# Kernel optimization log

Measured on AMD Instinct MI355X. Metric: run time of the kernel, lower is better.

Reference implementation:

```python
import jax, jax.numpy as jnp
import numpy as np

B, T, I, O, M = 64, 512, 256, 1024, 8
MS = O // M          # module_size
IM = I * M           # input_dim * num_modules


def setup_inputs() -> dict:
    key = jax.random.key(0)
    ks = jax.random.split(key, 6)
    s = 0.02
    return {
        "x": jax.random.normal(ks[0], (B, T, I), dtype=jnp.float32),
        "W_in": jax.random.normal(ks[1], (O, I), dtype=jnp.float32) * s,
        "b_in": jnp.zeros((O,), dtype=jnp.float32),
        "W_h": jax.random.normal(ks[2], (O, O), dtype=jnp.float32) * s,
        "W_ir": jax.random.normal(ks[3], (IM, I), dtype=jnp.float32) * s,
        "b_ir": jnp.zeros((IM,), dtype=jnp.float32),
        "W_hr": jax.random.normal(ks[4], (IM, IM), dtype=jnp.float32) * s,
        "module_periods": jnp.ones((M,), dtype=jnp.float32),
        "module_shifts": jnp.zeros((M,), dtype=jnp.float32),
    }


def reference(x, W_in, b_in, W_h, W_ir, b_ir, W_hr, module_periods, module_shifts):
    # x: [B, T, I]
    def step(carry, inp):
        h, x_pred = carry           # h: [B,O], x_pred: [B,IM]
        ti, xi = inp                # ti scalar float, xi: [B,I]
        acts = jnp.tanh(xi @ W_in.T + b_in + h @ W_h.T)            # [B,O]
        acts_rec = jnp.tanh(xi @ W_ir.T + b_ir + x_pred @ W_hr.T)  # [B,IM]
        m_xp = x_pred.reshape(B, M, I)
        # NOTE: nn.LogSoftmax() with no dim on a 3D tensor defaults to dim=0 (batch axis)
        surprisal = jax.nn.log_softmax(m_xp, axis=0) * xi[:, None, :]  # [B,M,I]
        mean_surprisal = surprisal.mean(-1)                            # [B,M]
        mp = mean_surprisal * module_periods                           # [B,M]
        gate = (jnp.sin(ti * mp + module_shifts) + 1.0) * 0.5          # [B,M]
        gate_full = jnp.repeat(gate, MS, axis=-1)                      # [B,O]
        y = (1.0 - gate_full) * acts + gate_full * h
        return (y, acts_rec), (y, mp)

    ts = jnp.arange(T, dtype=x.dtype)
    carry0 = (jnp.zeros((B, O), dtype=x.dtype), jnp.zeros((B, IM), dtype=x.dtype))
    (h_final, _), (ys, ps) = jax.lax.scan(step, carry0, (ts, jnp.swapaxes(x, 0, 1)))
    ys = jnp.swapaxes(ys, 0, 1)   # [B,T,O]
    ps = jnp.swapaxes(ps, 0, 1)   # [B,T,M]
    return ys, h_final, ps
```

## Files before the change

kernel.cpp:

```cpp
#include <hip/hip_runtime.h>
#include <hip/hip_fp16.h>

typedef _Float16 f16;
typedef f16 f16x8 __attribute__((ext_vector_type(8)));
typedef f16 f16x4 __attribute__((ext_vector_type(4)));
typedef float f32x4 __attribute__((ext_vector_type(4)));
typedef float f32x16 __attribute__((ext_vector_type(16)));

#define B_ 64
#define T_ 512
#define I_ 256
#define O_ 1024
#define M_ 8
#define IM_ 2048
#define NRECB 128
#define NB 192
#define THREADS 256

#define OFF_X16 4096ull
#define SZ_X16  ((unsigned long long)T_ * B_ * I_ * 2)
#define OFF_XP3 (OFF_X16 + SZ_X16)
#define SZ_XP3  (3ull * B_ * IM_ * 2)
#define OFF_H2  (OFF_XP3 + SZ_XP3)

#define LEAFA(i) ((i) * 16)
#define CENTA    128
#define FLAGA(i) (192 + (i) * 16)
#define LEAFB(i) (320 + (i) * 16)
#define CENTB    448
#define FLAGB(i) (512 + (i) * 16)

#define CMB_REC 147456
#define XPRAW   81920
#define CMB_ACT 114688
#define LSE_O   126976
#define PART_O  128000
#define GATE_O  129024
#define SMEM_SZ 159744

#define WAITV(N) asm volatile("s_waitcnt vmcnt(" #N ")" ::: "memory")
#define LGKM0    asm volatile("s_waitcnt lgkmcnt(0)" ::: "memory")
#define SCHEDB   __builtin_amdgcn_sched_barrier(0)
#define BARRIER  __builtin_amdgcn_s_barrier()

#define ISSUE_AX(BUF, P) asm volatile( \
    "global_load_dwordx4 %0, %8, off\n\t" \
    "global_load_dwordx4 %1, %8, off offset:32\n\t" \
    "global_load_dwordx4 %2, %8, off offset:64\n\t" \
    "global_load_dwordx4 %3, %8, off offset:96\n\t" \
    "global_load_dwordx4 %4, %8, off offset:128\n\t" \
    "global_load_dwordx4 %5, %8, off offset:160\n\t" \
    "global_load_dwordx4 %6, %8, off offset:192\n\t" \
    "global_load_dwordx4 %7, %8, off offset:224" \
    : "=&v"(abuf[BUF][0]), "=&v"(abuf[BUF][1]), "=&v"(abuf[BUF][2]), "=&v"(abuf[BUF][3]), \
      "=&v"(abuf[BUF][4]), "=&v"(abuf[BUF][5]), "=&v"(abuf[BUF][6]), "=&v"(abuf[BUF][7]) \
    : "v"(P) : "memory")

#define ISSUE_AS(BUF, P) asm volatile( \
    "global_load_dwordx4 %0, %8, off sc0 sc1\n\t" \
    "global_load_dwordx4 %1, %8, off offset:32 sc0 sc1\n\t" \
    "global_load_dwordx4 %2, %8, off offset:64 sc0 sc1\n\t" \
    "global_load_dwordx4 %3, %8, off offset:96 sc0 sc1\n\t" \
    "global_load_dwordx4 %4, %8, off offset:128 sc0 sc1\n\t" \
    "global_load_dwordx4 %5, %8, off offset:160 sc0 sc1\n\t" \
    "global_load_dwordx4 %6, %8, off offset:192 sc0 sc1\n\t" \
    "global_load_dwordx4 %7, %8, off offset:224 sc0 sc1" \
    : "=&v"(abuf[BUF][0]), "=&v"(abuf[BUF][1]), "=&v"(abuf[BUF][2]), "=&v"(abuf[BUF][3]), \
      "=&v"(abuf[BUF][4]), "=&v"(abuf[BUF][5]), "=&v"(abuf[BUF][6]), "=&v"(abuf[BUF][7]) \
    : "v"(P) : "memory")

#define ISSUE8P(ARR, P0,P1,P2,P3,P4,P5,P6,P7) asm volatile( \
    "global_load_dwordx4 %0, %8, off sc0 sc1\n\t" \
    "global_load_dwordx4 %1, %9, off sc0 sc1\n\t" \
    "global_load_dwordx4 %2, %10, off sc0 sc1\n\t" \
    "global_load_dwordx4 %3, %11, off sc0 sc1\n\t" \
    "global_load_dwordx4 %4, %12, off sc0 sc1\n\t" \
    "global_load_dwordx4 %5, %13, off sc0 sc1\n\t" \
    "global_load_dwordx4 %6, %14, off sc0 sc1\n\t" \
    "global_load_dwordx4 %7, %15, off sc0 sc1" \
    : "=&v"((ARR)[0]), "=&v"((ARR)[1]), "=&v"((ARR)[2]), "=&v"((ARR)[3]), \
      "=&v"((ARR)[4]), "=&v"((ARR)[5]), "=&v"((ARR)[6]), "=&v"((ARR)[7]) \
    : "v"(P0), "v"(P1), "v"(P2), "v"(P3), "v"(P4), "v"(P5), "v"(P6), "v"(P7) \
    : "memory")

#define CH(I, WN) do { \
    WAITV(WN); SCHEDB; \
    _Pragma("unroll") \
    for (int kb = 0; kb < 8; ++kb) { \
        f16x8 bf = *(const f16x8*)(smem + addrB[kb] + (I) * 256); \
        if (kb & 1) acc1 = __builtin_amdgcn_mfma_f32_32x32x16_f16(abuf[I][kb], bf, acc1, 0, 0, 0); \
        else        acc0 = __builtin_amdgcn_mfma_f32_32x32x16_f16(abuf[I][kb], bf, acc0, 0, 0, 0); \
    } \
} while (0)

__device__ __forceinline__ void st_coh_h(f16* p, float vf) {
    union { f16 h; short s; } u; u.h = (f16)vf;
    asm volatile("global_store_short %0, %1, off sc0 sc1" :: "v"(p), "v"((int)u.s) : "memory");
}

__device__ __forceinline__ float fast_tanh(float x) {
    float e = __expf(2.f * x);
    return 1.f - 2.f / (e + 1.f);
}

__device__ __forceinline__ unsigned ld_rlx(unsigned* p) {
    return __hip_atomic_load(p, __ATOMIC_RELAXED, __HIP_MEMORY_SCOPE_AGENT);
}

__device__ __forceinline__ void post_flags(unsigned* bar, int base, unsigned v) {
    #pragma unroll
    for (int i = 0; i < 8; ++i) {
        unsigned* rp = &bar[base + i * 16];
        asm volatile("global_store_dword %0, %1, off sc0 sc1" :: "v"(rp), "v"(v) : "memory");
    }
}

__device__ __forceinline__ void arriveA(unsigned* bar, int blk, int t) {
    unsigned old = __hip_atomic_fetch_add(&bar[LEAFA(blk & 7)], 1u, __ATOMIC_RELAXED, __HIP_MEMORY_SCOPE_AGENT);
    if (old % 16u == 15u) {
        unsigned r = __hip_atomic_fetch_add(&bar[CENTA], 1u, __ATOMIC_RELAXED, __HIP_MEMORY_SCOPE_AGENT);
        if ((r & 7u) == 7u) post_flags(bar, FLAGA(0), (unsigned)(t + 1));
    }
}
__device__ __forceinline__ void arriveB(unsigned* bar, int a, int t) {
    unsigned old = __hip_atomic_fetch_add(&bar[LEAFB(a & 7)], 1u, __ATOMIC_RELAXED, __HIP_MEMORY_SCOPE_AGENT);
    if ((old & 7u) == 7u) {
        unsigned r = __hip_atomic_fetch_add(&bar[CENTB], 1u, __ATOMIC_RELAXED, __HIP_MEMORY_SCOPE_AGENT);
        if ((r & 7u) == 7u) post_flags(bar, FLAGB(0), (unsigned)(t + 1));
    }
}

__global__ void init_kernel(const float* __restrict__ x, char* __restrict__ ws) {
    const int gid = blockIdx.x * 256 + threadIdx.x;
    if (blockIdx.x == 0) {
        for (int i = threadIdx.x; i < 1024; i += 256) ((unsigned*)ws)[i] = 0u;
    }
    f16* x16 = (f16*)(ws + OFF_X16);
    const int NQ = T_ * B_ * (I_ / 4);
    for (int q = gid; q < NQ; q += 256 * 256) {
        int t = q >> 12;
        int rem = q & 4095;
        int b = rem >> 6;
        int k4 = rem & 63;
        f32x4 v = *(const f32x4*)(x + ((size_t)b * T_ + t) * I_ + k4 * 4);
        f16x4 h;
        h[0] = (f16)v[0]; h[1] = (f16)v[1]; h[2] = (f16)v[2]; h[3] = (f16)v[3];
        *(f16x4*)(x16 + ((size_t)t * B_ + b) * I_ + k4 * 4) = h;
    }
    f16x8 z = {0, 0, 0, 0, 0, 0, 0, 0};
    f16* xp0 = (f16*)(ws + OFF_XP3);
    for (int e = gid * 8; e < B_ * IM_; e += 256 * 256 * 8) *(f16x8*)(xp0 + e) = z;
    f16* h0 = (f16*)(ws + OFF_H2);
    for (int e = gid * 8; e < B_ * O_; e += 256 * 256 * 8) *(f16x8*)(h0 + e) = z;
}

__global__ __launch_bounds__(THREADS, 1) void cwrnn_kernel(
    const float* __restrict__ x, const float* __restrict__ W_in, const float* __restrict__ b_in,
    const float* __restrict__ W_h, const float* __restrict__ W_ir, const float* __restrict__ b_ir,
    const float* __restrict__ W_hr, const float* __restrict__ periods, const float* __restrict__ shifts,
    float* __restrict__ out, char* __restrict__ ws)
{
    __shared__ __align__(16) char smem[SMEM_SZ];

    unsigned* bar = (unsigned*)ws;
    const int blk = blockIdx.x, tid = threadIdx.x;
    const int lane = tid & 63, w = tid >> 6;
    const int col = lane & 31, g = lane >> 5;

    float* ys = out;
    float* hfin = out + (size_t)B_ * T_ * O_;
    float* ps = hfin + (size_t)B_ * O_;

    if (blk < NRECB) {
        const int cg = blk >> 1, rh = blk & 1;
        const int j0 = cg * 32;
        const int row0 = rh * 32;
        const int arow = row0 + col;
        {
            const int j = tid & 31;
            const float* ra = W_ir + (size_t)(j0 + j) * I_;
            const float* rb = W_hr + (size_t)(j0 + j) * IM_ - 256;
            for (int u = (tid >> 5); u < 288; u += 8) {
                int k0 = u * 8;
                const float* s = (k0 < 256) ? (ra + k0) : (rb + k0);
                f32x4 lo = *(const f32x4*)s;
                f32x4 hi = *(const f32x4*)(s + 4);
                f16x8 v;
                #pragma unroll
                for (int e = 0; e < 4; ++e) { v[e] = (f16)lo[e]; v[e + 4] = (f16)hi[e]; }
                *(f16x8*)(smem + j * 4608 + ((u ^ (j & 15)) << 4)) = v;
            }
        }
        const float bir = b_ir[j0 + col];
        LGKM0; BARRIER;

        const int c0k = (w == 0) ? 0 : (w == 1) ? 5 : (w == 2) ? 10 : 14;
        int addrB[8];
        #pragma unroll
        for (int kb = 0; kb < 8; ++kb)
            addrB[kb] = col * 4608 + ((((kb << 1) + g) ^ (col & 15)) << 4) + c0k * 256;

        const char* xrow0 = (const char*)(ws + OFF_X16) + (size_t)arow * 512 + g * 16;
        f16* const xpB = (f16*)(ws + OFF_XP3);
        unsigned* fA = &bar[FLAGA(blk & 7)];
        unsigned* fB = &bar[FLAGB(blk & 7)];

        for (int t = 0; t < T_ - 1; ++t) {
            if (tid == 0) {
                while (1) {
                    int fa = (int)ld_rlx(fA);
                    int fb = (int)ld_rlx(fB);
                    if (fa >= t && fb >= t - 1) break;
                    __builtin_amdgcn_s_sleep(2);
                }
            }
            BARRIER;
            const int bi = t % 3;
            int bn = bi + 1; if (bn == 3) bn = 0;
            const f16* xpcur = xpB + (size_t)bi * B_ * IM_;
            f16* xpnxt = xpB + (size_t)bn * B_ * IM_;
            const char* sprow = (const char*)xpcur + (size_t)arow * 4096 + g * 16 - 512;
            const char* xrow = xrow0 + (size_t)t * 32768;

            f16x8 abuf[5][8];
            f32x16 acc0, acc1;
            #pragma unroll
            for (int r = 0; r < 16; ++r) { acc0[r] = 0.f; acc1[r] = 0.f; }

            if (w == 0) {
                ISSUE_AX(0, xrow); ISSUE_AX(1, (xrow + 256));
                ISSUE_AS(2, (sprow + 2 * 256)); ISSUE_AS(3, (sprow + 3 * 256)); ISSUE_AS(4, (sprow + 4 * 256));
                CH(0, 32); CH(1, 24); CH(2, 16); CH(3, 8); CH(4, 0);
            } else if (w == 1) {
                ISSUE_AS(0, (sprow + 5 * 256)); ISSUE_AS(1, (sprow + 6 * 256)); ISSUE_AS(2, (sprow + 7 * 256));
                ISSUE_AS(3, (sprow + 8 * 256)); ISSUE_AS(4, (sprow + 9 * 256));
                CH(0, 32); CH(1, 24); CH(2, 16); CH(3, 8); CH(4, 0);
            } else if (w == 2) {
                ISSUE_AS(0, (sprow + 10 * 256)); ISSUE_AS(1, (sprow + 11 * 256));
                ISSUE_AS(2, (sprow + 12 * 256)); ISSUE_AS(3, (sprow + 13 * 256));
                CH(0, 24); CH(1, 16); CH(2, 8); CH(3, 0);
            } else {
                ISSUE_AS(0, (sprow + 14 * 256)); ISSUE_AS(1, (sprow + 15 * 256));
                ISSUE_AS(2, (sprow + 16 * 256)); ISSUE_AS(3, (sprow + 17 * 256));
                CH(0, 24); CH(1, 16); CH(2, 8); CH(3, 0);
            }

            f32x16 accS;
            #pragma unroll
            for (int r = 0; r < 16; ++r) accS[r] = acc0[r] + acc1[r];
            if (w > 0) {
                char* cb = smem + CMB_REC + (w - 1) * 4096 + lane * 16;
                #pragma unroll
                for (int q = 0; q < 4; ++q) {
                    f32x4 v = { accS[q*4+0], accS[q*4+1], accS[q*4+2], accS[q*4+3] };
                    *(f32x4*)(cb + q * 1024) = v;
                }
            }
            LGKM0; BARRIER;
            if (w == 0) {
                #pragma unroll
                for (int wv = 0; wv < 3; ++wv) {
                    const char* cb = smem + CMB_REC + wv * 4096 + lane * 16;
                    #pragma unroll
                    for (int q = 0; q < 4; ++q) {
                        f32x4 v = *(const f32x4*)(cb + q * 1024);
                        accS[q*4+0] += v[0]; accS[q*4+1] += v[1];
                        accS[q*4+2] += v[2]; accS[q*4+3] += v[3];
                    }
                }
                #pragma unroll
                for (int r = 0; r < 16; ++r) {
                    int rloc = (r & 3) + ((r >> 2) << 3) + (g << 2);
                    st_coh_h(xpnxt + (size_t)(row0 + rloc) * IM_ + j0 + col, fast_tanh(accS[r] + bir));
                }
            }
            WAITV(0);
            BARRIER;
            if (tid == 0) arriveA(bar, blk, t);
        }
    } else {
        const int a = blk - NRECB;
        const int colg = a >> 1, rh = a & 1;
        const int m = colg >> 2;
        const int o0 = colg * 32;
        const int row0 = rh * 32;
        const int arow = row0 + col;
        {
            const int j = tid & 31;
            const float* ra = W_in + (size_t)(o0 + j) * I_;
            const float* rb = W_h + (size_t)(o0 + j) * O_ - 256;
            for (int u = (tid >> 5); u < 160; u += 8) {
                int k0 = u * 8;
                const float* s = (k0 < 256) ? (ra + k0) : (rb + k0);
                f32x4 lo = *(const f32x4*)s;
                f32x4 hi = *(const f32x4*)(s + 4);
                f16x8 v;
                #pragma unroll
                for (int e = 0; e < 4; ++e) { v[e] = (f16)lo[e]; v[e + 4] = (f16)hi[e]; }
                *(f16x8*)(smem + j * 2560 + ((u ^ (j & 15)) << 4)) = v;
            }
        }
        const float bin = b_in[o0 + col];
        const float per = periods[m], shf = shifts[m];
        LGKM0; BARRIER;

        const int c0k = (w == 0) ? 0 : (w == 1) ? 3 : (w == 2) ? 6 : 8;
        int addrB[8];
        #pragma unroll
        for (int kb = 0; kb < 8; ++kb)
            addrB[kb] = col * 2560 + ((((kb << 1) + g) ^ (col & 15)) << 4) + c0k * 256;

        char* xp_raw = smem + XPRAW;
        float* lse_lds = (float*)(smem + LSE_O);
        float* part_lds = (float*)(smem + PART_O);
        float* gate_lds = (float*)(smem + GATE_O);

        const char* xrow0 = (const char*)(ws + OFF_X16) + (size_t)arow * 512 + g * 16;
        const f16* xpB = (const f16*)(ws + OFF_XP3);
        f16* h2 = (f16*)(ws + OFF_H2);
        unsigned* fA = &bar[FLAGA(a & 7)];
        unsigned* fB = &bar[FLAGB(a & 7)];
        float hreg[16];
        #pragma unroll
        for (int r = 0; r < 16; ++r) hreg[r] = 0.f;

        const int s_ = tid - 128;
        const int cg2 = s_ & 31;
        const int r0s = (s_ >> 5) << 4;

        for (int t = 0; t < T_; ++t) {
            if (tid == 0) {
                while (1) {
                    int fa = (int)ld_rlx(fA);
                    int fb = (int)ld_rlx(fB);
                    if (fa >= t && fb >= t) break;
                    __builtin_amdgcn_s_sleep(2);
                }
            }
            BARRIER;
            const int bi = t % 3;
            const f16* xpcur = xpB + (size_t)bi * B_ * IM_;
            const f16* hcur = h2 + (size_t)(t & 1) * B_ * O_;
            f16* hnxt = h2 + (size_t)((t + 1) & 1) * B_ * O_;

            const char* sprow = (const char*)hcur + (size_t)arow * 2048 + g * 16 - 512;
            const char* xrow = xrow0 + (size_t)t * 32768;
            f16x8 abuf[3][8];
            f16x8 sregA[8], sregB[8];
            f32x16 acc0, acc1;
            #pragma unroll
            for (int r = 0; r < 16; ++r) { acc0[r] = 0.f; acc1[r] = 0.f; }

            if (w == 0) {
                ISSUE_AX(0, xrow); ISSUE_AX(1, (xrow + 256)); ISSUE_AS(2, (sprow + 2 * 256));
                CH(0, 16); CH(1, 8); CH(2, 0);
            } else if (w == 1) {
                ISSUE_AS(0, (sprow + 3 * 256)); ISSUE_AS(1, (sprow + 4 * 256)); ISSUE_AS(2, (sprow + 5 * 256));
                CH(0, 16); CH(1, 8); CH(2, 0);
            } else {
                const int ca = (w == 2) ? 6 : 8;
                ISSUE_AS(0, (sprow + ca * 256)); ISSUE_AS(1, (sprow + (ca + 1) * 256));
                const char* xb = (const char*)xpcur + (size_t)m * 512 + (size_t)cg2 * 16 + (size_t)r0s * 4096;
                ISSUE8P(sregA, xb, xb + 4096, xb + 2*4096, xb + 3*4096,
                               xb + 4*4096, xb + 5*4096, xb + 6*4096, xb + 7*4096);
                ISSUE8P(sregB, (xb + 8*4096), xb + 9*4096, xb + 10*4096, xb + 11*4096,
                               xb + 12*4096, xb + 13*4096, xb + 14*4096, xb + 15*4096);
                CH(0, 24); CH(1, 16);
                WAITV(0); SCHEDB;
                #pragma unroll
                for (int k = 0; k < 8; ++k) {
                    int b0 = r0s + k;
                    *(f16x8*)(xp_raw + (size_t)b0 * 512 + ((cg2 ^ (b0 & 7)) << 4)) = sregA[k];
                    int b1 = r0s + 8 + k;
                    *(f16x8*)(xp_raw + (size_t)b1 * 512 + ((cg2 ^ (b1 & 7)) << 4)) = sregB[k];
                }
            }

            f32x16 accS;
            #pragma unroll
            for (int r = 0; r < 16; ++r) accS[r] = acc0[r] + acc1[r];
            if (w > 0) {
                char* cb = smem + CMB_ACT + (w - 1) * 4096 + lane * 16;
                #pragma unroll
                for (int q = 0; q < 4; ++q) {
                    f32x4 v = { accS[q*4+0], accS[q*4+1], accS[q*4+2], accS[q*4+3] };
                    *(f32x4*)(cb + q * 1024) = v;
                }
            }
            LGKM0; BARRIER;
            {
                int i = tid;
                int gq = i >> 3, r2 = (i & 7) * 2;
                float s = 0.f;
                #pragma unroll 8
                for (int b = 0; b < B_; ++b)
                    s += __expf((float)*(const f16*)(xp_raw + b * 512 + ((gq ^ (b & 7)) << 4) + r2));
                lse_lds[i] = __logf(s);
            }
            if (w == 0) {
                #pragma unroll
                for (int wv = 0; wv < 3; ++wv) {
                    const char* cb = smem + CMB_ACT + wv * 4096 + lane * 16;
                    #pragma unroll
                    for (int q = 0; q < 4; ++q) {
                        f32x4 v = *(const f32x4*)(cb + q * 1024);
                        accS[q*4+0] += v[0]; accS[q*4+1] += v[1];
                        accS[q*4+2] += v[2]; accS[q*4+3] += v[3];
                    }
                }
            }
            LGKM0; BARRIER;
            {
                int b = tid >> 2, q = tid & 3;
                const float* xr = x + ((size_t)b * T_ + t) * I_ + q * 64;
                float s = 0.f;
                #pragma unroll
                for (int k = 0; k < 8; ++k) {
                    f16x8 xp8 = *(const f16x8*)(xp_raw + (size_t)b * 512 + ((((q << 3) + k) ^ (b & 7)) << 4));
                    f32x4 xa = *(const f32x4*)(xr + k * 8);
                    f32x4 xb2 = *(const f32x4*)(xr + k * 8 + 4);
                    #pragma unroll
                    for (int jj = 0; jj < 4; ++jj)
                        s += ((float)xp8[jj] - lse_lds[(q << 6) + (k << 3) + jj]) * xa[jj];
                    #pragma unroll
                    for (int jj = 0; jj < 4; ++jj)
                        s += ((float)xp8[jj + 4] - lse_lds[(q << 6) + (k << 3) + 4 + jj]) * xb2[jj];
                }
                part_lds[tid] = s;
            }
            LGKM0; BARRIER;
            if (tid < B_) {
                float s = part_lds[tid * 4] + part_lds[tid * 4 + 1] + part_lds[tid * 4 + 2] + part_lds[tid * 4 + 3];
                float mp = (s * (1.f / 256.f)) * per;
                gate_lds[tid] = 0.5f * (sinf((float)t * mp + shf) + 1.f);
                if ((a & 7) == 0) ps[((size_t)tid * T_ + t) * M_ + m] = mp;
            }
            LGKM0; BARRIER;
            if (w == 0) {
                #pragma unroll
                for (int r = 0; r < 16; ++r) {
                    int rloc = (r & 3) + ((r >> 2) << 3) + (g << 2);
                    int row = row0 + rloc;
                    float gt = gate_lds[row];
                    float av = fast_tanh(accS[r] + bin);
                    float y = (1.f - gt) * av + gt * hreg[r];
                    hreg[r] = y;
                    st_coh_h(hnxt + (size_t)row * O_ + o0 + col, y);
                    ys[((size_t)row * T_ + t) * O_ + o0 + col] = y;
                    if (t == T_ - 1) hfin[(size_t)row * O_ + o0 + col] = y;
                }
            }
            WAITV(0);
            BARRIER;
            if (tid == 0) arriveB(bar, a, t);
        }
    }
}

extern "C" void kernel_launch(void* const* d_in, const int* in_sizes, int n_in,
                              void* d_out, int out_size, void* d_ws, size_t ws_size,
                              hipStream_t stream) {
    const float* x    = (const float*)d_in[0];
    const float* W_in = (const float*)d_in[1];
    const float* b_in = (const float*)d_in[2];
    const float* W_h  = (const float*)d_in[3];
    const float* W_ir = (const float*)d_in[4];
    const float* b_ir = (const float*)d_in[5];
    const float* W_hr = (const float*)d_in[6];
    const float* per  = (const float*)d_in[7];
    const float* shf  = (const float*)d_in[8];

    hipLaunchKernelGGL(init_kernel, dim3(256), dim3(256), 0, stream,
                       x, (char*)d_ws);
    hipLaunchKernelGGL(cwrnn_kernel, dim3(NB), dim3(THREADS), 0, stream,
                       x, W_in, b_in, W_h, W_ir, b_ir, W_hr, per, shf,
                       (float*)d_out, (char*)d_ws);
}
```

Before: 5.471 ms.

## Replicate per-step state into per-XCD buffers to read with L2-cached loads

Each block reads its XCD ID at startup and registers itself, then the blocks on each XCD cooperatively copy the current x_pred and h state into a per-XCD replica buffer every timestep. A per-XCD counter barrier guards the copy. The GEMM operand loads then read the replica with sc0 only instead of sc0 sc1, so they can hit the local L2 rather than going to memory coherently. This adds a copy phase and an extra intra-XCD barrier per step, and the recurrence loop now runs T iterations so recurrent blocks take part in the copying.

```diff
diff --git a/kernel.cpp b/kernel.cpp
--- a/kernel.cpp
+++ b/kernel.cpp
@@ -17,11 +17,13 @@
 #define NB 192
 #define THREADS 256
 
-#define OFF_X16 4096ull
-#define SZ_X16  ((unsigned long long)T_ * B_ * I_ * 2)
-#define OFF_XP3 (OFF_X16 + SZ_X16)
-#define SZ_XP3  (3ull * B_ * IM_ * 2)
-#define OFF_H2  (OFF_XP3 + SZ_XP3)
+#define OFF_X16 8192ull
+#define OFF_XP3 16785408ull
+#define OFF_H2  17571840ull
+#define OFF_REP 17833984ull
+#define REP_XCD 786432ull
+#define REP_PAR 393216ull
+#define REP_H   262144ull
 
 #define LEAFA(i) ((i) * 16)
 #define CENTA    128
@@ -29,6 +31,11 @@
 #define LEAFB(i) (320 + (i) * 16)
 #define CENTB    448
 #define FLAGB(i) (512 + (i) * 16)
+#define REGC     640
+#define NR_(i)   (656 + (i) * 16)
+#define NA_(i)   (784 + (i) * 16)
+#define XBX_(i)  (912 + (i) * 16)
+#define XBH_(i)  (1040 + (i) * 16)
 
 #define CMB_REC 147456
 #define XPRAW   81920
@@ -36,7 +43,8 @@
 #define LSE_O   126976
 #define PART_O  128000
 #define GATE_O  129024
-#define SMEM_SZ 159744
+#define META_O  159744
+#define SMEM_SZ 159808
 
 #define WAITV(N) asm volatile("s_waitcnt vmcnt(" #N ")" ::: "memory")
 #define LGKM0    asm volatile("s_waitcnt lgkmcnt(0)" ::: "memory")
@@ -56,28 +64,28 @@
       "=&v"(abuf[BUF][4]), "=&v"(abuf[BUF][5]), "=&v"(abuf[BUF][6]), "=&v"(abuf[BUF][7]) \
     : "v"(P) : "memory")
 
-#define ISSUE_AS(BUF, P) asm volatile( \
-    "global_load_dwordx4 %0, %8, off sc0 sc1\n\t" \
-    "global_load_dwordx4 %1, %8, off offset:32 sc0 sc1\n\t" \
-    "global_load_dwordx4 %2, %8, off offset:64 sc0 sc1\n\t" \
-    "global_load_dwordx4 %3, %8, off offset:96 sc0 sc1\n\t" \
-    "global_load_dwordx4 %4, %8, off offset:128 sc0 sc1\n\t" \
-    "global_load_dwordx4 %5, %8, off offset:160 sc0 sc1\n\t" \
-    "global_load_dwordx4 %6, %8, off offset:192 sc0 sc1\n\t" \
-    "global_load_dwordx4 %7, %8, off offset:224 sc0 sc1" \
+#define ISSUE_A0(BUF, P) asm volatile( \
+    "global_load_dwordx4 %0, %8, off sc0\n\t" \
+    "global_load_dwordx4 %1, %8, off offset:32 sc0\n\t" \
+    "global_load_dwordx4 %2, %8, off offset:64 sc0\n\t" \
+    "global_load_dwordx4 %3, %8, off offset:96 sc0\n\t" \
+    "global_load_dwordx4 %4, %8, off offset:128 sc0\n\t" \
+    "global_load_dwordx4 %5, %8, off offset:160 sc0\n\t" \
+    "global_load_dwordx4 %6, %8, off offset:192 sc0\n\t" \
+    "global_load_dwordx4 %7, %8, off offset:224 sc0" \
     : "=&v"(abuf[BUF][0]), "=&v"(abuf[BUF][1]), "=&v"(abuf[BUF][2]), "=&v"(abuf[BUF][3]), \
       "=&v"(abuf[BUF][4]), "=&v"(abuf[BUF][5]), "=&v"(abuf[BUF][6]), "=&v"(abuf[BUF][7]) \
     : "v"(P) : "memory")
 
-#define ISSUE8P(ARR, P0,P1,P2,P3,P4,P5,P6,P7) asm volatile( \
-    "global_load_dwordx4 %0, %8, off sc0 sc1\n\t" \
-    "global_load_dwordx4 %1, %9, off sc0 sc1\n\t" \
-    "global_load_dwordx4 %2, %10, off sc0 sc1\n\t" \
-    "global_load_dwordx4 %3, %11, off sc0 sc1\n\t" \
-    "global_load_dwordx4 %4, %12, off sc0 sc1\n\t" \
-    "global_load_dwordx4 %5, %13, off sc0 sc1\n\t" \
-    "global_load_dwordx4 %6, %14, off sc0 sc1\n\t" \
-    "global_load_dwordx4 %7, %15, off sc0 sc1" \
+#define ISSUE8P0(ARR, P0,P1,P2,P3,P4,P5,P6,P7) asm volatile( \
+    "global_load_dwordx4 %0, %8, off sc0\n\t" \
+    "global_load_dwordx4 %1, %9, off sc0\n\t" \
+    "global_load_dwordx4 %2, %10, off sc0\n\t" \
+    "global_load_dwordx4 %3, %11, off sc0\n\t" \
+    "global_load_dwordx4 %4, %12, off sc0\n\t" \
+    "global_load_dwordx4 %5, %13, off sc0\n\t" \
+    "global_load_dwordx4 %6, %14, off sc0\n\t" \
+    "global_load_dwordx4 %7, %15, off sc0" \
     : "=&v"((ARR)[0]), "=&v"((ARR)[1]), "=&v"((ARR)[2]), "=&v"((ARR)[3]), \
       "=&v"((ARR)[4]), "=&v"((ARR)[5]), "=&v"((ARR)[6]), "=&v"((ARR)[7]) \
     : "v"(P0), "v"(P1), "v"(P2), "v"(P3), "v"(P4), "v"(P5), "v"(P6), "v"(P7) \
@@ -106,6 +114,9 @@
 __device__ __forceinline__ unsigned ld_rlx(unsigned* p) {
     return __hip_atomic_load(p, __ATOMIC_RELAXED, __HIP_MEMORY_SCOPE_AGENT);
 }
+__device__ __forceinline__ unsigned rmw_add(unsigned* p) {
+    return __hip_atomic_fetch_add(p, 1u, __ATOMIC_RELAXED, __HIP_MEMORY_SCOPE_AGENT);
+}
 
 __device__ __forceinline__ void post_flags(unsigned* bar, int base, unsigned v) {
     #pragma unroll
@@ -116,24 +127,46 @@
 }
 
 __device__ __forceinline__ void arriveA(unsigned* bar, int blk, int t) {
-    unsigned old = __hip_atomic_fetch_add(&bar[LEAFA(blk & 7)], 1u, __ATOMIC_RELAXED, __HIP_MEMORY_SCOPE_AGENT);
+    unsigned old = rmw_add(&bar[LEAFA(blk & 7)]);
     if (old % 16u == 15u) {
-        unsigned r = __hip_atomic_fetch_add(&bar[CENTA], 1u, __ATOMIC_RELAXED, __HIP_MEMORY_SCOPE_AGENT);
+        unsigned r = rmw_add(&bar[CENTA]);
         if ((r & 7u) == 7u) post_flags(bar, FLAGA(0), (unsigned)(t + 1));
     }
 }
 __device__ __forceinline__ void arriveB(unsigned* bar, int a, int t) {
-    unsigned old = __hip_atomic_fetch_add(&bar[LEAFB(a & 7)], 1u, __ATOMIC_RELAXED, __HIP_MEMORY_SCOPE_AGENT);
+    unsigned old = rmw_add(&bar[LEAFB(a & 7)]);
     if ((old & 7u) == 7u) {
-        unsigned r = __hip_atomic_fetch_add(&bar[CENTB], 1u, __ATOMIC_RELAXED, __HIP_MEMORY_SCOPE_AGENT);
+        unsigned r = rmw_add(&bar[CENTB]);
         if ((r & 7u) == 7u) post_flags(bar, FLAGB(0), (unsigned)(t + 1));
+    }
+}
+
+__device__ __forceinline__ void copy_slices(const char* src, char* dst,
+                                            int r, int c, int nslices, int tid) {
+    for (int s = r; s < nslices; s += c) {
+        const char* p0 = src + (size_t)s * 16384 + tid * 16;
+        char* d0 = dst + (size_t)s * 16384 + tid * 16;
+        f16x8 v0, v1, v2, v3;
+        asm volatile(
+            "global_load_dwordx4 %0, %4, off sc0 sc1\n\t"
+            "global_load_dwordx4 %1, %5, off sc0 sc1\n\t"
+            "global_load_dwordx4 %2, %6, off sc0 sc1\n\t"
+            "global_load_dwordx4 %3, %7, off sc0 sc1"
+            : "=&v"(v0), "=&v"(v1), "=&v"(v2), "=&v"(v3)
+            : "v"(p0), "v"(p0 + 4096), "v"(p0 + 8192), "v"(p0 + 12288)
+            : "memory");
+        WAITV(0); SCHEDB;
+        *(f16x8*)(d0) = v0;
+        *(f16x8*)(d0 + 4096) = v1;
+        *(f16x8*)(d0 + 8192) = v2;
+        *(f16x8*)(d0 + 12288) = v3;
     }
 }
 
 __global__ void init_kernel(const float* __restrict__ x, char* __restrict__ ws) {
     const int gid = blockIdx.x * 256 + threadIdx.x;
     if (blockIdx.x == 0) {
-        for (int i = threadIdx.x; i < 1024; i += 256) ((unsigned*)ws)[i] = 0u;
+        for (int i = threadIdx.x; i < 2048; i += 256) ((unsigned*)ws)[i] = 0u;
     }
     f16* x16 = (f16*)(ws + OFF_X16);
     const int NQ = T_ * B_ * (I_ / 4);
@@ -171,7 +204,37 @@
     float* hfin = out + (size_t)B_ * T_ * O_;
     float* ps = hfin + (size_t)B_ * O_;
 
-    if (blk < NRECB) {
+    int* meta = (int*)(smem + META_O);
+    if (tid == 0) {
+        unsigned xcdv;
+        asm volatile("s_getreg_b32 %0, hwreg(HW_REG_XCC_ID)" : "=s"(xcdv));
+        xcdv &= 7u;
+        unsigned rnk;
+        if (blk < NRECB) rnk = rmw_add(&bar[NR_(xcdv)]);
+        else             rnk = rmw_add(&bar[NA_(xcdv)]);
+        WAITV(0);
+        rmw_add(&bar[REGC]);
+        while (ld_rlx(&bar[REGC]) < (unsigned)NB) __builtin_amdgcn_s_sleep(8);
+        meta[0] = (int)xcdv;
+        meta[1] = (int)rnk;
+        meta[2] = (int)ld_rlx(&bar[NR_(xcdv)]);
+        meta[3] = (int)ld_rlx(&bar[NA_(xcdv)]);
+    }
+    LGKM0; BARRIER;
+    const int xcd = meta[0], rank = meta[1], nR = meta[2], nA = meta[3];
+    const bool isREC = (blk < NRECB);
+    const bool doXP = isREC || (nR == 0);
+    const bool doH  = (!isREC) || (nA == 0);
+    const int cX = (nR > 0) ? nR : nA;
+    const int cH = (nA > 0) ? nA : nR;
+    const bool needFbT = isREC && (nA == 0);
+    char* rep = ws + OFF_REP + (size_t)xcd * REP_XCD;
+    unsigned* xbX = &bar[XBX_(xcd)];
+    unsigned* xbH = &bar[XBH_(xcd)];
+    f16* const xpB = (f16*)(ws + OFF_XP3);
+    f16* h2 = (f16*)(ws + OFF_H2);
+
+    if (isREC) {
         const int cg = blk >> 1, rh = blk & 1;
         const int j0 = cg * 32;
         const int row0 = rh * 32;
@@ -201,80 +264,94 @@
             addrB[kb] = col * 4608 + ((((kb << 1) + g) ^ (col & 15)) << 4) + c0k * 256;
 
         const char* xrow0 = (const char*)(ws + OFF_X16) + (size_t)arow * 512 + g * 16;
-        f16* const xpB = (f16*)(ws + OFF_XP3);
         unsigned* fA = &bar[FLAGA(blk & 7)];
         unsigned* fB = &bar[FLAGB(blk & 7)];
 
-        for (int t = 0; t < T_ - 1; ++t) {
+        for (int t = 0; t < T_; ++t) {
             if (tid == 0) {
                 while (1) {
                     int fa = (int)ld_rlx(fA);
                     int fb = (int)ld_rlx(fB);
-                    if (fa >= t && fb >= t - 1) break;
+                    if (fa >= t && fb >= t - 1 && (!needFbT || fb >= t)) break;
                     __builtin_amdgcn_s_sleep(2);
                 }
             }
             BARRIER;
             const int bi = t % 3;
             int bn = bi + 1; if (bn == 3) bn = 0;
-            const f16* xpcur = xpB + (size_t)bi * B_ * IM_;
-            f16* xpnxt = xpB + (size_t)bn * B_ * IM_;
-            const char* sprow = (const char*)xpcur + (size_t)arow * 4096 + g * 16 - 512;
-            const char* xrow = xrow0 + (size_t)t * 32768;
-
-            f16x8 abuf[5][8];
-            f32x16 acc0, acc1;
-            #pragma unroll
-            for (int r = 0; r < 16; ++r) { acc0[r] = 0.f; acc1[r] = 0.f; }
-
-            if (w == 0) {
-                ISSUE_AX(0, xrow); ISSUE_AX(1, (xrow + 256));
-                ISSUE_AS(2, (sprow + 2 * 256)); ISSUE_AS(3, (sprow + 3 * 256)); ISSUE_AS(4, (sprow + 4 * 256));
-                CH(0, 32); CH(1, 24); CH(2, 16); CH(3, 8); CH(4, 0);
-            } else if (w == 1) {
-                ISSUE_AS(0, (sprow + 5 * 256)); ISSUE_AS(1, (sprow + 6 * 256)); ISSUE_AS(2, (sprow + 7 * 256));
-                ISSUE_AS(3, (sprow + 8 * 256)); ISSUE_AS(4, (sprow + 9 * 256));
-                CH(0, 32); CH(1, 24); CH(2, 16); CH(3, 8); CH(4, 0);
-            } else if (w == 2) {
-                ISSUE_AS(0, (sprow + 10 * 256)); ISSUE_AS(1, (sprow + 11 * 256));
-                ISSUE_AS(2, (sprow + 12 * 256)); ISSUE_AS(3, (sprow + 13 * 256));
-                CH(0, 24); CH(1, 16); CH(2, 8); CH(3, 0);
-            } else {
-                ISSUE_AS(0, (sprow + 14 * 256)); ISSUE_AS(1, (sprow + 15 * 256));
-                ISSUE_AS(2, (sprow + 16 * 256)); ISSUE_AS(3, (sprow + 17 * 256));
-                CH(0, 24); CH(1, 16); CH(2, 8); CH(3, 0);
-            }
-
-            f32x16 accS;
-            #pragma unroll
-            for (int r = 0; r < 16; ++r) accS[r] = acc0[r] + acc1[r];
-            if (w > 0) {
-                char* cb = smem + CMB_REC + (w - 1) * 4096 + lane * 16;
-                #pragma unroll
-                for (int q = 0; q < 4; ++q) {
-                    f32x4 v = { accS[q*4+0], accS[q*4+1], accS[q*4+2], accS[q*4+3] };
-                    *(f32x4*)(cb + q * 1024) = v;
-                }
-            }
-            LGKM0; BARRIER;
-            if (w == 0) {
-                #pragma unroll
-                for (int wv = 0; wv < 3; ++wv) {
-                    const char* cb = smem + CMB_REC + wv * 4096 + lane * 16;
+            char* repP = rep + (size_t)(t & 1) * REP_PAR;
+            if (doXP) copy_slices((const char*)(xpB + (size_t)bi * B_ * IM_), repP, rank, cX, 16, tid);
+            if (doH)  copy_slices((const char*)(h2 + (size_t)(t & 1) * B_ * O_), repP + REP_H, rank, cH, 8, tid);
+            WAITV(0);
+            BARRIER;
+            if (tid == 0) {
+                if (doXP) rmw_add(xbX);
+                if (doH)  rmw_add(xbH);
+            }
+            if (t < T_ - 1) {
+                if (tid == 0) {
+                    unsigned tgt = (unsigned)(cX * (t + 1));
+                    while (ld_rlx(xbX) < tgt) __builtin_amdgcn_s_sleep(1);
+                }
+                BARRIER;
+                f16* xpnxt = xpB + (size_t)bn * B_ * IM_;
+                const char* sprow = (const char*)repP + (size_t)arow * 4096 + g * 16 - 512;
+                const char* xrow = xrow0 + (size_t)t * 32768;
+
+                f16x8 abuf[5][8];
+                f32x16 acc0, acc1;
+                #pragma unroll
+                for (int r = 0; r < 16; ++r) { acc0[r] = 0.f; acc1[r] = 0.f; }
+
+                if (w == 0) {
+                    ISSUE_AX(0, xrow); ISSUE_AX(1, (xrow + 256));
+                    ISSUE_A0(2, (sprow + 2 * 256)); ISSUE_A0(3, (sprow + 3 * 256)); ISSUE_A0(4, (sprow + 4 * 256));
+                    CH(0, 32); CH(1, 24); CH(2, 16); CH(3, 8); CH(4, 0);
+                } else if (w == 1) {
+                    ISSUE_A0(0, (sprow + 5 * 256)); ISSUE_A0(1, (sprow + 6 * 256)); ISSUE_A0(2, (sprow + 7 * 256));
+                    ISSUE_A0(3, (sprow + 8 * 256)); ISSUE_A0(4, (sprow + 9 * 256));
+                    CH(0, 32); CH(1, 24); CH(2, 16); CH(3, 8); CH(4, 0);
+                } else if (w == 2) {
+                    ISSUE_A0(0, (sprow + 10 * 256)); ISSUE_A0(1, (sprow + 11 * 256));
+                    ISSUE_A0(2, (sprow + 12 * 256)); ISSUE_A0(3, (sprow + 13 * 256));
+                    CH(0, 24); CH(1, 16); CH(2, 8); CH(3, 0);
+                } else {
+                    ISSUE_A0(0, (sprow + 14 * 256)); ISSUE_A0(1, (sprow + 15 * 256));
+                    ISSUE_A0(2, (sprow + 16 * 256)); ISSUE_A0(3, (sprow + 17 * 256));
+                    CH(0, 24); CH(1, 16); CH(2, 8); CH(3, 0);
+                }
+
+                f32x16 accS;
+                #pragma unroll
+                for (int r = 0; r < 16; ++r) accS[r] = acc0[r] + acc1[r];
+                if (w > 0) {
+                    char* cb = smem + CMB_REC + (w - 1) * 4096 + lane * 16;
                     #pragma unroll
                     for (int q = 0; q < 4; ++q) {
-                        f32x4 v = *(const f32x4*)(cb + q * 1024);
-                        accS[q*4+0] += v[0]; accS[q*4+1] += v[1];
-                        accS[q*4+2] += v[2]; accS[q*4+3] += v[3];
+                        f32x4 v = { accS[q*4+0], accS[q*4+1], accS[q*4+2], accS[q*4+3] };
+                        *(f32x4*)(cb + q * 1024) = v;
                     }
                 }
-                #pragma unroll
-                for (int r = 0; r < 16; ++r) {
-                    int rloc = (r & 3) + ((r >> 2) << 3) + (g << 2);
-                    st_coh_h(xpnxt + (size_t)(row0 + rloc) * IM_ + j0 + col, fast_tanh(accS[r] + bir));
-                }
-            }
-            WAITV(0);
+                LGKM0; BARRIER;
+                if (w == 0) {
+                    #pragma unroll
+                    for (int wv = 0; wv < 3; ++wv) {
+                        const char* cb = smem + CMB_REC + wv * 4096 + lane * 16;
+                        #pragma unroll
+                        for (int q = 0; q < 4; ++q) {
+                            f32x4 v = *(const f32x4*)(cb + q * 1024);
+                            accS[q*4+0] += v[0]; accS[q*4+1] += v[1];
+                            accS[q*4+2] += v[2]; accS[q*4+3] += v[3];
+                        }
+                    }
+                    #pragma unroll
+                    for (int r = 0; r < 16; ++r) {
+                        int rloc = (r & 3) + ((r >> 2) << 3) + (g << 2);
+                        st_coh_h(xpnxt + (size_t)(row0 + rloc) * IM_ + j0 + col, fast_tanh(accS[r] + bir));
+                    }
+                }
+                WAITV(0);
+            }
             BARRIER;
             if (tid == 0) arriveA(bar, blk, t);
         }
@@ -316,8 +393,6 @@
         float* gate_lds = (float*)(smem + GATE_O);
 
         const char* xrow0 = (const char*)(ws + OFF_X16) + (size_t)arow * 512 + g * 16;
-        const f16* xpB = (const f16*)(ws + OFF_XP3);
-        f16* h2 = (f16*)(ws + OFF_H2);
         unsigned* fA = &bar[FLAGA(a & 7)];
         unsigned* fB = &bar[FLAGB(a & 7)];
         float hreg[16];
@@ -339,11 +414,20 @@
             }
             BARRIER;
             const int bi = t % 3;
-            const f16* xpcur = xpB + (size_t)bi * B_ * IM_;
-            const f16* hcur = h2 + (size_t)(t & 1) * B_ * O_;
+            char* repP = rep + (size_t)(t & 1) * REP_PAR;
+            if (doXP) copy_slices((const char*)(xpB + (size_t)bi * B_ * IM_), repP, rank, cX, 16, tid);
+            if (doH)  copy_slices((const char*)(h2 + (size_t)(t & 1) * B_ * O_), repP + REP_H, rank, cH, 8, tid);
+            WAITV(0);
+            BARRIER;
+            if (tid == 0) {
+                if (doXP) rmw_add(xbX);
+                if (doH)  rmw_add(xbH);
+                unsigned tX = (unsigned)(cX * (t + 1)), tH = (unsigned)(cH * (t + 1));
+                while (ld_rlx(xbX) < tX || ld_rlx(xbH) < tH) __builtin_amdgcn_s_sleep(1);
+            }
+            BARRIER;
             f16* hnxt = h2 + (size_t)((t + 1) & 1) * B_ * O_;
-
-            const char* sprow = (const char*)hcur + (size_t)arow * 2048 + g * 16 - 512;
+            const char* sprow = (const char*)repP + REP_H + (size_t)arow * 2048 + g * 16 - 512;
             const char* xrow = xrow0 + (size_t)t * 32768;
             f16x8 abuf[3][8];
             f16x8 sregA[8], sregB[8];
@@ -352,18 +436,18 @@
             for (int r = 0; r < 16; ++r) { acc0[r] = 0.f; acc1[r] = 0.f; }
 
             if (w == 0) {
-                ISSUE_AX(0, xrow); ISSUE_AX(1, (xrow + 256)); ISSUE_AS(2, (sprow + 2 * 256));
+                ISSUE_AX(0, xrow); ISSUE_AX(1, (xrow + 256)); ISSUE_A0(2, (sprow + 2 * 256));
                 CH(0, 16); CH(1, 8); CH(2, 0);
             } else if (w == 1) {
-                ISSUE_AS(0, (sprow + 3 * 256)); ISSUE_AS(1, (sprow + 4 * 256)); ISSUE_AS(2, (sprow + 5 * 256));
+                ISSUE_A0(0, (sprow + 3 * 256)); ISSUE_A0(1, (sprow + 4 * 256)); ISSUE_A0(2, (sprow + 5 * 256));
                 CH(0, 16); CH(1, 8); CH(2, 0);
             } else {
                 const int ca = (w == 2) ? 6 : 8;
-                ISSUE_AS(0, (sprow + ca * 256)); ISSUE_AS(1, (sprow + (ca + 1) * 256));
-                const char* xb = (const char*)xpcur + (size_t)m * 512 + (size_t)cg2 * 16 + (size_t)r0s * 4096;
-                ISSUE8P(sregA, xb, xb + 4096, xb + 2*4096, xb + 3*4096,
+                ISSUE_A0(0, (sprow + ca * 256)); ISSUE_A0(1, (sprow + (ca + 1) * 256));
+                const char* xb = (const char*)repP + (size_t)m * 512 + (size_t)cg2 * 16 + (size_t)r0s * 4096;
+                ISSUE8P0(sregA, xb, xb + 4096, xb + 2*4096, xb + 3*4096,
                                xb + 4*4096, xb + 5*4096, xb + 6*4096, xb + 7*4096);
-                ISSUE8P(sregB, (xb + 8*4096), xb + 9*4096, xb + 10*4096, xb + 11*4096,
+                ISSUE8P0(sregB, (xb + 8*4096), xb + 9*4096, xb + 10*4096, xb + 11*4096,
                                xb + 12*4096, xb + 13*4096, xb + 14*4096, xb + 15*4096);
                 CH(0, 24); CH(1, 16);
                 WAITV(0); SCHEDB;
```

Result: slower. 6.366 ms (+16.4%).

## Replace atomic tree barriers with per-block flag slots polled by wavefronts

Applied to the files above, without the earlier changes.

Removes the hierarchical atomic-counter barrier (leaf/center counters plus broadcast flags). Each block now writes its own progress flag slot after its stores, and consumers poll only the slots they depend on, with one wave checking 64 slots via ballot. The x_pred ring grows from three to four buffers so recurrent blocks can run further ahead of the activation blocks. This cuts out the atomic round trips and the trailing block-wide barrier on the critical path per timestep, at the cost of more polling traffic and a reliance on the memory ordering of the coherent stores.

```diff
diff --git a/kernel.cpp b/kernel.cpp
--- a/kernel.cpp
+++ b/kernel.cpp
@@ -17,18 +17,13 @@
 #define NB 192
 #define THREADS 256
 
-#define OFF_X16 4096ull
-#define SZ_X16  ((unsigned long long)T_ * B_ * I_ * 2)
-#define OFF_XP3 (OFF_X16 + SZ_X16)
-#define SZ_XP3  (3ull * B_ * IM_ * 2)
-#define OFF_H2  (OFF_XP3 + SZ_XP3)
-
-#define LEAFA(i) ((i) * 16)
-#define CENTA    128
-#define FLAGA(i) (192 + (i) * 16)
-#define LEAFB(i) (320 + (i) * 16)
-#define CENTB    448
-#define FLAGB(i) (512 + (i) * 16)
+#define OFF_X16 16384ull
+#define SZ_X16  16777216ull
+#define OFF_XP4 (OFF_X16 + SZ_X16)
+#define OFF_H2  (OFF_XP4 + 4ull * B_ * IM_ * 2)
+
+#define RECF_D(rh) (1024 + (rh) * 256)
+#define ACTF_D     1536
 
 #define CMB_REC 147456
 #define XPRAW   81920
@@ -103,37 +98,20 @@
     return 1.f - 2.f / (e + 1.f);
 }
 
-__device__ __forceinline__ unsigned ld_rlx(unsigned* p) {
-    return __hip_atomic_load(p, __ATOMIC_RELAXED, __HIP_MEMORY_SCOPE_AGENT);
-}
-
-__device__ __forceinline__ void post_flags(unsigned* bar, int base, unsigned v) {
-    #pragma unroll
-    for (int i = 0; i < 8; ++i) {
-        unsigned* rp = &bar[base + i * 16];
-        asm volatile("global_store_dword %0, %1, off sc0 sc1" :: "v"(rp), "v"(v) : "memory");
-    }
-}
-
-__device__ __forceinline__ void arriveA(unsigned* bar, int blk, int t) {
-    unsigned old = __hip_atomic_fetch_add(&bar[LEAFA(blk & 7)], 1u, __ATOMIC_RELAXED, __HIP_MEMORY_SCOPE_AGENT);
-    if (old % 16u == 15u) {
-        unsigned r = __hip_atomic_fetch_add(&bar[CENTA], 1u, __ATOMIC_RELAXED, __HIP_MEMORY_SCOPE_AGENT);
-        if ((r & 7u) == 7u) post_flags(bar, FLAGA(0), (unsigned)(t + 1));
-    }
-}
-__device__ __forceinline__ void arriveB(unsigned* bar, int a, int t) {
-    unsigned old = __hip_atomic_fetch_add(&bar[LEAFB(a & 7)], 1u, __ATOMIC_RELAXED, __HIP_MEMORY_SCOPE_AGENT);
-    if ((old & 7u) == 7u) {
-        unsigned r = __hip_atomic_fetch_add(&bar[CENTB], 1u, __ATOMIC_RELAXED, __HIP_MEMORY_SCOPE_AGENT);
-        if ((r & 7u) == 7u) post_flags(bar, FLAGB(0), (unsigned)(t + 1));
-    }
+__device__ __forceinline__ int ld_flag(const unsigned* p) {
+    int v;
+    asm volatile("global_load_dword %0, %1, off sc0 sc1" : "=v"(v) : "v"(p) : "memory");
+    WAITV(0);
+    return v;
+}
+__device__ __forceinline__ void st_flag(unsigned* p, int v) {
+    asm volatile("global_store_dword %0, %1, off sc0 sc1" :: "v"(p), "v"(v) : "memory");
 }
 
 __global__ void init_kernel(const float* __restrict__ x, char* __restrict__ ws) {
     const int gid = blockIdx.x * 256 + threadIdx.x;
     if (blockIdx.x == 0) {
-        for (int i = threadIdx.x; i < 1024; i += 256) ((unsigned*)ws)[i] = 0u;
+        for (int i = threadIdx.x; i < 4096; i += 256) ((unsigned*)ws)[i] = 0u;
     }
     f16* x16 = (f16*)(ws + OFF_X16);
     const int NQ = T_ * B_ * (I_ / 4);
@@ -148,7 +126,7 @@
         *(f16x4*)(x16 + ((size_t)t * B_ + b) * I_ + k4 * 4) = h;
     }
     f16x8 z = {0, 0, 0, 0, 0, 0, 0, 0};
-    f16* xp0 = (f16*)(ws + OFF_XP3);
+    f16* xp0 = (f16*)(ws + OFF_XP4);
     for (int e = gid * 8; e < B_ * IM_; e += 256 * 256 * 8) *(f16x8*)(xp0 + e) = z;
     f16* h0 = (f16*)(ws + OFF_H2);
     for (int e = gid * 8; e < B_ * O_; e += 256 * 256 * 8) *(f16x8*)(h0 + e) = z;
@@ -170,6 +148,9 @@
     float* ys = out;
     float* hfin = out + (size_t)B_ * T_ * O_;
     float* ps = hfin + (size_t)B_ * O_;
+
+    f16* const xpB = (f16*)(ws + OFF_XP4);
+    f16* h2 = (f16*)(ws + OFF_H2);
 
     if (blk < NRECB) {
         const int cg = blk >> 1, rh = blk & 1;
@@ -201,22 +182,19 @@
             addrB[kb] = col * 4608 + ((((kb << 1) + g) ^ (col & 15)) << 4) + c0k * 256;
 
         const char* xrow0 = (const char*)(ws + OFF_X16) + (size_t)arow * 512 + g * 16;
-        f16* const xpB = (f16*)(ws + OFF_XP3);
-        unsigned* fA = &bar[FLAGA(blk & 7)];
-        unsigned* fB = &bar[FLAGB(blk & 7)];
+        unsigned* myslot = bar + RECF_D(rh) + cg * 4;
 
         for (int t = 0; t < T_ - 1; ++t) {
-            if (tid == 0) {
-                while (1) {
-                    int fa = (int)ld_rlx(fA);
-                    int fb = (int)ld_rlx(fB);
-                    if (fa >= t && fb >= t - 1) break;
-                    __builtin_amdgcn_s_sleep(2);
-                }
+            if (w == 0) {
+                const unsigned* p = bar + RECF_D(rh) + lane * 4;
+                while (__ballot(ld_flag(p) >= t) != ~0ull) __builtin_amdgcn_s_sleep(4);
+            } else if (w == 1) {
+                const unsigned* p = bar + ACTF_D + lane * 4;
+                const int tgt = t - 2;
+                while (__ballot(ld_flag(p) >= tgt) != ~0ull) __builtin_amdgcn_s_sleep(4);
             }
             BARRIER;
-            const int bi = t % 3;
-            int bn = bi + 1; if (bn == 3) bn = 0;
+            const int bi = t & 3, bn = (t + 1) & 3;
             const f16* xpcur = xpB + (size_t)bi * B_ * IM_;
             f16* xpnxt = xpB + (size_t)bn * B_ * IM_;
             const char* sprow = (const char*)xpcur + (size_t)arow * 4096 + g * 16 - 512;
@@ -273,10 +251,9 @@
                     int rloc = (r & 3) + ((r >> 2) << 3) + (g << 2);
                     st_coh_h(xpnxt + (size_t)(row0 + rloc) * IM_ + j0 + col, fast_tanh(accS[r] + bir));
                 }
-            }
-            WAITV(0);
-            BARRIER;
-            if (tid == 0) arriveA(bar, blk, t);
+                WAITV(0);
+                if (tid == 0) st_flag(myslot, t + 1);
+            }
         }
     } else {
         const int a = blk - NRECB;
@@ -316,10 +293,7 @@
         float* gate_lds = (float*)(smem + GATE_O);
 
         const char* xrow0 = (const char*)(ws + OFF_X16) + (size_t)arow * 512 + g * 16;
-        const f16* xpB = (const f16*)(ws + OFF_XP3);
-        f16* h2 = (f16*)(ws + OFF_H2);
-        unsigned* fA = &bar[FLAGA(a & 7)];
-        unsigned* fB = &bar[FLAGB(a & 7)];
+        unsigned* myslot = bar + ACTF_D + (rh * 32 + colg) * 4;
         float hreg[16];
         #pragma unroll
         for (int r = 0; r < 16; ++r) hreg[r] = 0.f;
@@ -329,16 +303,18 @@
         const int r0s = (s_ >> 5) << 4;
 
         for (int t = 0; t < T_; ++t) {
-            if (tid == 0) {
-                while (1) {
-                    int fa = (int)ld_rlx(fA);
-                    int fb = (int)ld_rlx(fB);
-                    if (fa >= t && fb >= t) break;
-                    __builtin_amdgcn_s_sleep(2);
-                }
+            if (w == 0) {
+                const unsigned* p = bar + RECF_D(0) + lane * 4;
+                while (__ballot(ld_flag(p) >= t) != ~0ull) __builtin_amdgcn_s_sleep(4);
+            } else if (w == 1) {
+                const unsigned* p = bar + RECF_D(1) + lane * 4;
+                while (__ballot(ld_flag(p) >= t) != ~0ull) __builtin_amdgcn_s_sleep(4);
+            } else if (w == 2) {
+                const unsigned* p = bar + ACTF_D + (rh * 32 + (lane & 31)) * 4;
+                while (__ballot((lane < 32) ? (ld_flag(p) >= t) : 1) != ~0ull) __builtin_amdgcn_s_sleep(4);
             }
             BARRIER;
-            const int bi = t % 3;
+            const int bi = t & 3;
             const f16* xpcur = xpB + (size_t)bi * B_ * IM_;
             const f16* hcur = h2 + (size_t)(t & 1) * B_ * O_;
             f16* hnxt = h2 + (size_t)((t + 1) & 1) * B_ * O_;
@@ -449,10 +425,9 @@
                     ys[((size_t)row * T_ + t) * O_ + o0 + col] = y;
                     if (t == T_ - 1) hfin[(size_t)row * O_ + o0 + col] = y;
                 }
-            }
-            WAITV(0);
-            BARRIER;
-            if (tid == 0) arriveB(bar, a, t);
+                WAITV(0);
+                if (tid == 0) st_flag(myslot, t + 1);
+            }
         }
     }
 }
```

Result: no change. 5.484 ms (+0.2%).
